# Kernel optimization log

Hardware: AMD Instinct MI355X
Metric: run time of the kernel (lower is better)

## Reference

```python
import jax, jax.numpy as jnp
import numpy as np

N_NODES = 50000
N_EDGES = 800000
N_GRAPHS = 64
IN_C = 64
HID = 64
NEG_SLOPE = 0.2  # PyG GATConv default


def setup_inputs() -> dict:
    key = jax.random.key(0)
    ks = jax.random.split(key, 12)
    x = jax.random.normal(ks[0], (N_NODES, IN_C), dtype=jnp.float32)
    edge_index = jax.random.randint(ks[1], (2, N_EDGES), 0, N_NODES, dtype=jnp.int64)
    batch = jnp.sort(jax.random.randint(ks[2], (N_NODES,), 0, N_GRAPHS, dtype=jnp.int64))
    s = 1.0 / np.sqrt(IN_C)
    sh = 1.0 / np.sqrt(HID)
    W = jax.random.uniform(ks[3], (IN_C, HID), jnp.float32, -s, s)
    att_src = jax.random.uniform(ks[4], (HID,), jnp.float32, -sh, sh)
    att_dst = jax.random.uniform(ks[5], (HID,), jnp.float32, -sh, sh)
    bias_gat = jnp.zeros((HID,), jnp.float32)
    w1 = jax.random.uniform(ks[6], (HID, HID), jnp.float32, -sh, sh)
    b1 = jax.random.uniform(ks[7], (HID,), jnp.float32, -sh, sh)
    w2 = jax.random.uniform(ks[8], (HID, 1), jnp.float32, -sh, sh)
    b2 = jax.random.uniform(ks[9], (1,), jnp.float32, -sh, sh)
    return {"x": x, "edge_index": edge_index, "batch": batch, "W": W,
            "att_src": att_src, "att_dst": att_dst, "bias_gat": bias_gat,
            "w1": w1, "b1": b1, "w2": w2, "b2": b2}


def _gat_conv(x, edge_index, W, att_src, att_dst, bias_gat):
    N = x.shape[0]
    # add self-loops (PyG default)
    loops = jnp.arange(N, dtype=edge_index.dtype)
    src = jnp.concatenate([edge_index[0], loops])  # message source j
    dst = jnp.concatenate([edge_index[1], loops])  # message target i
    h = x @ W                                      # [N, HID]
    a_s = h @ att_src                              # [N]
    a_d = h @ att_dst                              # [N]
    e = jax.nn.leaky_relu(a_s[src] + a_d[dst], negative_slope=NEG_SLOPE)  # [E+N]
    # segment softmax over incoming edges of each target node
    m = jax.ops.segment_max(e, dst, num_segments=N)
    ex = jnp.exp(e - m[dst])
    denom = jax.ops.segment_sum(ex, dst, num_segments=N)
    alpha = ex / denom[dst]
    out = jax.ops.segment_sum(h[src] * alpha[:, None], dst, num_segments=N)
    return out + bias_gat


def reference(x, edge_index, batch, W, att_src, att_dst, bias_gat, w1, b1, w2, b2):
    h = jax.nn.relu(_gat_conv(x, edge_index, W, att_src, att_dst, bias_gat))
    # global mean pool over each graph
    sums = jax.ops.segment_sum(h, batch, num_segments=N_GRAPHS)          # [G, HID]
    cnt = jax.ops.segment_sum(jnp.ones((h.shape[0],), h.dtype), batch,
                              num_segments=N_GRAPHS)
    pooled = sums / jnp.maximum(cnt, 1.0)[:, None]
    z = jax.nn.relu(pooled @ w1 + b1)
    z = z @ w2 + b2
    return jax.nn.sigmoid(z)  # [G, 1]
```

## Files before the change

### kernel.cpp

```cpp
#include <hip/hip_runtime.h>
#include <hip/hip_bf16.h>

#define NN 50000
#define NE 800000
#define NG 64
#define HID 64
#define NEG 0.2f
#define NPW 64
#define NBUCK 196
#define CHUNK 2048
#define KC_CAP 6144

__device__ __forceinline__ unsigned short f2bf(float f) {
    unsigned int u = __float_as_uint(f);
    unsigned int r = (u + 0x7FFF + ((u >> 16) & 1)) >> 16;
    return (unsigned short)r;
}
__device__ __forceinline__ float bf2f(unsigned short b) {
    return __uint_as_float(((unsigned int)b) << 16);
}

__global__ __launch_bounds__(256)
void k_xw(const float* __restrict__ x, const float* __restrict__ W,
          const float* __restrict__ att_s, const float* __restrict__ att_d,
          unsigned short* __restrict__ hb, float* __restrict__ as_, float* __restrict__ ad_,
          int* __restrict__ gcur) {
    __shared__ __align__(16) float sW[64][64];
    __shared__ __align__(16) float sxT[64][68];
    int t = threadIdx.x;
    if (blockIdx.x == 0 && t < NBUCK) gcur[t] = 0;
    int r0 = blockIdx.x * 64;
    for (int i = t; i < 4096; i += 256) sW[i >> 6][i & 63] = W[i];
    for (int i = t; i < 4096; i += 256) {
        int r = i >> 6, c = i & 63;
        int gr = r0 + r; if (gr >= NN) gr = NN - 1;
        sxT[c][r] = x[(size_t)gr * 64 + c];
    }
    __syncthreads();

    int tx = t & 15, ty = t >> 4;
    float4 asv = ((const float4*)att_s)[tx];
    float4 adv = ((const float4*)att_d)[tx];

    float acc[4][4] = {};
    #pragma unroll
    for (int k = 0; k < 64; ++k) {
        float4 a = *(const float4*)&sxT[k][4 * ty];
        float4 b = *(const float4*)&sW[k][4 * tx];
        float av[4] = {a.x, a.y, a.z, a.w};
        float bv[4] = {b.x, b.y, b.z, b.w};
        #pragma unroll
        for (int i = 0; i < 4; ++i)
            #pragma unroll
            for (int j = 0; j < 4; ++j)
                acc[i][j] += av[i] * bv[j];
    }

    #pragma unroll
    for (int i = 0; i < 4; ++i) {
        int r = r0 + 4 * ty + i;
        if (r < NN) {
            ushort4 hv;
            hv.x = f2bf(acc[i][0]); hv.y = f2bf(acc[i][1]);
            hv.z = f2bf(acc[i][2]); hv.w = f2bf(acc[i][3]);
            *(ushort4*)&hb[(size_t)r * 64 + 4 * tx] = hv;
            float ps = acc[i][0]*asv.x + acc[i][1]*asv.y + acc[i][2]*asv.z + acc[i][3]*asv.w;
            float pd = acc[i][0]*adv.x + acc[i][1]*adv.y + acc[i][2]*adv.z + acc[i][3]*adv.w;
            #pragma unroll
            for (int m = 1; m <= 8; m <<= 1) {
                ps += __shfl_xor(ps, m, 64);
                pd += __shfl_xor(pd, m, 64);
            }
            if (tx == 0) { as_[r] = ps; ad_[r] = pd; }
        }
    }
}

__global__ __launch_bounds__(256)
void k_bucket(const int* __restrict__ src, const int* __restrict__ dst,
              int* __restrict__ gcur, int* __restrict__ ebuf) {
    __shared__ int lhist[256], lscan[256], loff[256], lcur[256], gbase[256];
    __shared__ int lsort[CHUNK];
    __shared__ unsigned char lbuck[CHUNK];
    int t = threadIdx.x;
    int base = blockIdx.x * CHUNK;
    int cnt = NE - base; if (cnt > CHUNK) cnt = CHUNK; if (cnt < 0) cnt = 0;

    int ds[8], ss[8];
    int nv = 0;
    #pragma unroll
    for (int j = 0; j < 8; ++j) {
        int e = base + j * 256 + t;
        if (e < NE) { ds[nv] = dst[e]; ss[nv] = src[e]; ++nv; }
    }
    lhist[t] = 0;
    __syncthreads();
    for (int j = 0; j < nv; ++j) atomicAdd(&lhist[ds[j] >> 8], 1);
    __syncthreads();
    lscan[t] = lhist[t];
    __syncthreads();
    for (int off = 1; off < 256; off <<= 1) {
        int u = (t >= off) ? lscan[t - off] : 0;
        __syncthreads();
        lscan[t] += u;
        __syncthreads();
    }
    loff[t] = lscan[t] - lhist[t];
    lcur[t] = 0;
    __syncthreads();
    for (int j = 0; j < nv; ++j) {
        int b = ds[j] >> 8;
        int r = atomicAdd(&lcur[b], 1);
        int slot = loff[b] + r;
        lsort[slot] = (ss[j] << 8) | (ds[j] & 255);
        lbuck[slot] = (unsigned char)b;
    }
    if (t < NBUCK) {
        int c = lhist[t];
        gbase[t] = c ? atomicAdd(&gcur[t], c) : 0;
    }
    __syncthreads();
    for (int i = t; i < cnt; i += 256) {
        int b = lbuck[i];
        ebuf[b * KC_CAP + gbase[b] + (i - loff[b])] = lsort[i];
    }
}

__global__ __launch_bounds__(256)
void k_csr(const int* __restrict__ gcur, const int* __restrict__ ebuf,
           int* __restrict__ csr, int* __restrict__ cursor, int* __restrict__ deg) {
    __shared__ int lhist[256], lscan[256], loff[256], lcur[256], bscan[256];
    __shared__ int lsrc[KC_CAP];
    int t = threadIdx.x;
    int b = blockIdx.x;

    bscan[t] = (t < NBUCK) ? gcur[t] : 0;
    __syncthreads();
    for (int off = 1; off < 256; off <<= 1) {
        int u = (t >= off) ? bscan[t - off] : 0;
        __syncthreads();
        bscan[t] += u;
        __syncthreads();
    }
    int sz = gcur[b];
    int gb = bscan[b] - sz;
    const int* seg = ebuf + b * KC_CAP;

    lhist[t] = 0;
    __syncthreads();
    for (int i = t; i < sz; i += 256)
        atomicAdd(&lhist[seg[i] & 255], 1);
    __syncthreads();
    lscan[t] = lhist[t];
    __syncthreads();
    for (int off = 1; off < 256; off <<= 1) {
        int u = (t >= off) ? lscan[t - off] : 0;
        __syncthreads();
        lscan[t] += u;
        __syncthreads();
    }
    loff[t] = lscan[t] - lhist[t];
    lcur[t] = 0;
    __syncthreads();
    for (int i = t; i < sz; i += 256) {
        int w = seg[i];
        int dl = w & 255;
        int r = atomicAdd(&lcur[dl], 1);
        lsrc[loff[dl] + r] = w >> 8;
    }
    __syncthreads();
    for (int i = t; i < sz; i += 256)
        csr[gb + i] = lsrc[i];
    int d = b * 256 + t;
    if (d < NN) {
        deg[d] = lhist[t];
        cursor[d] = gb + loff[t] + lhist[t];
    }
}

__global__ __launch_bounds__(256)
void k_gather(const int* __restrict__ csr, const int* __restrict__ cursor,
              const int* __restrict__ deg, const unsigned short* __restrict__ hb,
              const float* __restrict__ as_, const float* __restrict__ ad_,
              const float* __restrict__ bias, float* __restrict__ g,
              float* __restrict__ poolz) {
    int t = threadIdx.x;
    if (blockIdx.x == 0) {
        for (int i = t; i < NG * HID + NG; i += 256) poolz[i] = 0.f;
    }
    int wave = t >> 6, lane = t & 63;
    int d = blockIdx.x * 4 + wave;
    if (d >= NN) return;
    int cend = cursor[d];
    int nd   = deg[d];
    int cbeg = cend - nd;
    float adv = ad_[d];
    float e0 = as_[d] + adv;
    e0 = e0 >= 0.f ? e0 : NEG * e0;
    float ex0 = __expf(e0);
    float den = ex0;
    float acc = bf2f(hb[(size_t)d * 64 + lane]) * ex0;

    for (int c0 = 0; c0 < nd; c0 += 16) {
        int rem = nd - c0; if (rem > 16) rem = 16;
        int ci = cbeg + c0 + (lane & 15);
        if (ci >= cend) ci = cend - 1;
        int   myidx = csr[ci];
        float myas  = as_[myidx];
        if (rem == 16) {
            #pragma unroll
            for (int j = 0; j < 16; ++j) {
                int   s = __shfl(myidx, j, 16);
                float a = __shfl(myas,  j, 16);
                float av = a + adv;
                av = av >= 0.f ? av : NEG * av;
                float ex = __expf(av);
                den += ex;
                acc += bf2f(hb[(size_t)s * 64 + lane]) * ex;
            }
        } else {
            for (int j = 0; j < rem; ++j) {
                int   s = __shfl(myidx, j, 16);
                float a = __shfl(myas,  j, 16);
                float av = a + adv;
                av = av >= 0.f ? av : NEG * av;
                float ex = __expf(av);
                den += ex;
                acc += bf2f(hb[(size_t)s * 64 + lane]) * ex;
            }
        }
    }
    g[(size_t)d * 64 + lane] = fmaxf(acc / den + bias[lane], 0.f);
}

__global__ __launch_bounds__(256)
void k_node(const float* __restrict__ g, const int* __restrict__ batch,
            float* __restrict__ pooled, float* __restrict__ cnt) {
    int t = threadIdx.x;
    int wave = t >> 6, lane = t & 63;
    int n0 = (blockIdx.x * 4 + wave) * NPW;
    if (n0 >= NN) return;
    int n1 = n0 + NPW; if (n1 > NN) n1 = NN;
    float acc = 0.f, c = 0.f;
    int cur = batch[n0];
    for (int n = n0; n < n1; ++n) {
        int gr = batch[n];
        if (gr != cur) {
            atomicAdd(&pooled[cur * 64 + lane], acc);
            if (lane == 0) atomicAdd(&cnt[cur], c);
            acc = 0.f; c = 0.f; cur = gr;
        }
        acc += g[(size_t)n * 64 + lane];
        c += 1.f;
    }
    atomicAdd(&pooled[cur * 64 + lane], acc);
    if (lane == 0) atomicAdd(&cnt[cur], c);
}

__global__ __launch_bounds__(256)
void k_final(const float* __restrict__ pooled, const float* __restrict__ cnt,
             const float* __restrict__ w1, const float* __restrict__ b1,
             const float* __restrict__ w2, const float* __restrict__ b2,
             float* __restrict__ out) {
    __shared__ float sp[64][65];
    __shared__ float sz[64][65];
    int t = threadIdx.x;
    for (int i = t; i < 4096; i += 256) {
        int g = i >> 6, c = i & 63;
        sp[g][c] = pooled[i] / fmaxf(cnt[g], 1.0f);
    }
    __syncthreads();
    for (int i = t; i < 4096; i += 256) {
        int g = i >> 6, c = i & 63;
        float acc = b1[c];
        #pragma unroll
        for (int k = 0; k < 64; ++k) acc += sp[g][k] * w1[k * 64 + c];
        sz[g][c] = fmaxf(acc, 0.f);
    }
    __syncthreads();
    if (t < 64) {
        float acc = b2[0];
        #pragma unroll
        for (int c = 0; c < 64; ++c) acc += sz[t][c] * w2[c];
        out[t] = 1.f / (1.f + __expf(-acc));
    }
}

extern "C" void kernel_launch(void* const* d_in, const int* in_sizes, int n_in,
                              void* d_out, int out_size, void* d_ws, size_t ws_size,
                              hipStream_t stream) {
    const float* x     = (const float*)d_in[0];
    const int*   ei    = (const int*)d_in[1];
    const int*   batch = (const int*)d_in[2];
    const float* W     = (const float*)d_in[3];
    const float* att_s = (const float*)d_in[4];
    const float* att_d = (const float*)d_in[5];
    const float* bias  = (const float*)d_in[6];
    const float* w1    = (const float*)d_in[7];
    const float* b1    = (const float*)d_in[8];
    const float* w2    = (const float*)d_in[9];
    const float* b2    = (const float*)d_in[10];
    float* out = (float*)d_out;

    const int* src = ei;
    const int* dst = ei + NE;

    unsigned short* hb = (unsigned short*)d_ws;
    float* as_    = (float*)(hb + (size_t)NN * HID);
    float* ad_    = as_ + NN;
    float* g      = ad_ + NN;
    float* pooled = g + (size_t)NN * HID;
    float* cntp   = pooled + NG * HID;
    int*   deg    = (int*)(cntp + NG);
    int*   cursor = deg + NN;
    int*   csr    = cursor + NN;
    int*   gcur   = csr + NE;
    int*   ebuf   = (int*)g;

    k_xw<<<(NN + 63) / 64, 256, 0, stream>>>(x, W, att_s, att_d, hb, as_, ad_, gcur);

    k_bucket<<<(NE + CHUNK - 1) / CHUNK, 256, 0, stream>>>(src, dst, gcur, ebuf);
    k_csr<<<NBUCK, 256, 0, stream>>>(gcur, ebuf, csr, cursor, deg);

    k_gather<<<(NN + 3) / 4, 256, 0, stream>>>(csr, cursor, deg, hb, as_, ad_, bias, g, pooled);

    k_node<<<(NN / (4 * NPW)) + 1, 256, 0, stream>>>(g, batch, pooled, cntp);

    k_final<<<1, 256, 0, stream>>>(pooled, cntp, w1, b1, w2, b2, out);
}
```

Measured before the change: 142.7 us.

## Process eight edges per wave concurrently with 16-byte bf16 row loads in gather

The gather kernel now splits each 64-lane wave into 8 groups of 8 lanes. Each group handles a different incoming edge and each lane loads 8 bf16 features at once with a uint4 load, instead of the whole wave walking edges one at a time with 2-byte loads per lane. Partial accumulators and denominators are then combined across groups with xor shuffles, and group 0 writes the output with float4 stores. The aim is more memory-level parallelism and fewer, wider loads for the random row gathers, at the cost of more registers and a reduction step at the end.

```diff
diff --git a/kernel.cpp b/kernel.cpp
--- a/kernel.cpp
+++ b/kernel.cpp
@@ -16,8 +16,11 @@
     unsigned int r = (u + 0x7FFF + ((u >> 16) & 1)) >> 16;
     return (unsigned short)r;
 }
-__device__ __forceinline__ float bf2f(unsigned short b) {
-    return __uint_as_float(((unsigned int)b) << 16);
+__device__ __forceinline__ float bf_lo(unsigned int p) {
+    return __uint_as_float(p << 16);
+}
+__device__ __forceinline__ float bf_hi(unsigned int p) {
+    return __uint_as_float(p & 0xFFFF0000u);
 }
 
 __global__ __launch_bounds__(256)
@@ -191,46 +194,68 @@
     int wave = t >> 6, lane = t & 63;
     int d = blockIdx.x * 4 + wave;
     if (d >= NN) return;
+    int grp = lane >> 3;
+    int cc  = lane & 7;
     int cend = cursor[d];
     int nd   = deg[d];
     int cbeg = cend - nd;
     float adv = ad_[d];
-    float e0 = as_[d] + adv;
-    e0 = e0 >= 0.f ? e0 : NEG * e0;
-    float ex0 = __expf(e0);
-    float den = ex0;
-    float acc = bf2f(hb[(size_t)d * 64 + lane]) * ex0;
-
-    for (int c0 = 0; c0 < nd; c0 += 16) {
-        int rem = nd - c0; if (rem > 16) rem = 16;
-        int ci = cbeg + c0 + (lane & 15);
-        if (ci >= cend) ci = cend - 1;
-        int   myidx = csr[ci];
-        float myas  = as_[myidx];
-        if (rem == 16) {
-            #pragma unroll
-            for (int j = 0; j < 16; ++j) {
-                int   s = __shfl(myidx, j, 16);
-                float a = __shfl(myas,  j, 16);
-                float av = a + adv;
-                av = av >= 0.f ? av : NEG * av;
-                float ex = __expf(av);
-                den += ex;
-                acc += bf2f(hb[(size_t)s * 64 + lane]) * ex;
-            }
-        } else {
-            for (int j = 0; j < rem; ++j) {
-                int   s = __shfl(myidx, j, 16);
-                float a = __shfl(myas,  j, 16);
-                float av = a + adv;
-                av = av >= 0.f ? av : NEG * av;
-                float ex = __expf(av);
-                den += ex;
-                acc += bf2f(hb[(size_t)s * 64 + lane]) * ex;
-            }
-        }
-    }
-    g[(size_t)d * 64 + lane] = fmaxf(acc / den + bias[lane], 0.f);
+
+    float acc[8] = {};
+    float den = 0.f;
+
+    {
+        float e0 = as_[d] + adv;
+        e0 = e0 >= 0.f ? e0 : NEG * e0;
+        float ex0 = (grp == 0) ? __expf(e0) : 0.f;
+        den += ex0;
+        uint4 v = *(const uint4*)&hb[(size_t)d * 64 + 8 * cc];
+        acc[0] += bf_lo(v.x) * ex0;  acc[1] += bf_hi(v.x) * ex0;
+        acc[2] += bf_lo(v.y) * ex0;  acc[3] += bf_hi(v.y) * ex0;
+        acc[4] += bf_lo(v.z) * ex0;  acc[5] += bf_hi(v.z) * ex0;
+        acc[6] += bf_lo(v.w) * ex0;  acc[7] += bf_hi(v.w) * ex0;
+    }
+
+    for (int c0 = 0; c0 < nd; c0 += 8) {
+        int  e  = c0 + grp;
+        bool ok = e < nd;
+        int  ci = cbeg + (ok ? e : (nd - 1));
+        int    s = csr[ci];
+        float  a = as_[s];
+        float av = a + adv;
+        av = av >= 0.f ? av : NEG * av;
+        float ex = ok ? __expf(av) : 0.f;
+        den += ex;
+        uint4 v = *(const uint4*)&hb[(size_t)s * 64 + 8 * cc];
+        acc[0] += bf_lo(v.x) * ex;  acc[1] += bf_hi(v.x) * ex;
+        acc[2] += bf_lo(v.y) * ex;  acc[3] += bf_hi(v.y) * ex;
+        acc[4] += bf_lo(v.z) * ex;  acc[5] += bf_hi(v.z) * ex;
+        acc[6] += bf_lo(v.w) * ex;  acc[7] += bf_hi(v.w) * ex;
+    }
+
+    #pragma unroll
+    for (int m = 8; m <= 32; m <<= 1) {
+        den += __shfl_xor(den, m, 64);
+        #pragma unroll
+        for (int k = 0; k < 8; ++k) acc[k] += __shfl_xor(acc[k], m, 64);
+    }
+
+    if (grp == 0) {
+        float inv = 1.f / den;
+        float4 b0 = ((const float4*)bias)[2 * cc];
+        float4 b1 = ((const float4*)bias)[2 * cc + 1];
+        float4 o0, o1;
+        o0.x = fmaxf(acc[0] * inv + b0.x, 0.f);
+        o0.y = fmaxf(acc[1] * inv + b0.y, 0.f);
+        o0.z = fmaxf(acc[2] * inv + b0.z, 0.f);
+        o0.w = fmaxf(acc[3] * inv + b0.w, 0.f);
+        o1.x = fmaxf(acc[4] * inv + b1.x, 0.f);
+        o1.y = fmaxf(acc[5] * inv + b1.y, 0.f);
+        o1.z = fmaxf(acc[6] * inv + b1.z, 0.f);
+        o1.w = fmaxf(acc[7] * inv + b1.w, 0.f);
+        *(float4*)&g[(size_t)d * 64 + 8 * cc]     = o0;
+        *(float4*)&g[(size_t)d * 64 + 8 * cc + 4] = o1;
+    }
 }
 
 __global__ __launch_bounds__(256)
```

New measurement: 133.3 us. 6.5% less time.
